# Kernel tuning notes

Hardware: AMD Instinct MI355X
Metric: run time of the kernel (lower is better)

Reference implementation:

```python
import jax, jax.numpy as jnp
import numpy as np

N_NODES = 100000
F_DIM = 128      # graph.num_node_features
TE_DIM = 32      # te_emb_dim
D = F_DIM + TE_DIM  # attention embed_dim = 160
B = 4096         # number of target nodes (batched python loop)
K = 64           # candidates per target
TAU = 1.0
THRESHOLD = 0.2
EPS = 1e-10


def setup_inputs() -> dict:
    key = jax.random.key(0)
    ks = jax.random.split(key, 16)
    inp = {
        "x": jax.random.normal(ks[0], (N_NODES, F_DIM), dtype=jnp.float32),
        "target_node_ids": jax.random.randint(ks[1], (B,), 0, N_NODES),
        "target_node_times": jax.random.randint(ks[2], (B,), 1, 10000),
        "neighbor_ids": jax.random.randint(ks[3], (B, K), 0, N_NODES),
        "edge_time": jax.random.randint(ks[4], (B, K), 0, 10000),
        "edge_weight": jax.random.uniform(ks[5], (B, K), dtype=jnp.float32),
        "gumbel_u": jax.random.uniform(ks[6], (B, K), dtype=jnp.float32),
        # TemporalEncoding params: te(t) = cos(t * w + b)
        "te_w": jax.random.normal(ks[7], (TE_DIM,), dtype=jnp.float32),
        "te_b": jax.random.normal(ks[8], (TE_DIM,), dtype=jnp.float32),
        # MultiheadAttention params (packed qkv like torch)
        "in_proj_w": jax.random.normal(ks[9], (3 * D, D), dtype=jnp.float32) / np.sqrt(D),
        "in_proj_b": jnp.zeros((3 * D,), dtype=jnp.float32),
        "out_w": jax.random.normal(ks[10], (D, D), dtype=jnp.float32) / np.sqrt(D),
        "out_b": jnp.zeros((D,), dtype=jnp.float32),
        # MLP: Linear(D+1 -> 1) + LeakyReLU
        "mlp_w": jax.random.normal(ks[11], (D + 1,), dtype=jnp.float32) / np.sqrt(D + 1),
        "mlp_b": jnp.zeros((1,), dtype=jnp.float32),
    }
    return inp


def reference(x, target_node_ids, target_node_times, neighbor_ids, edge_time,
              edge_weight, gumbel_u, te_w, te_b, in_proj_w, in_proj_b,
              out_w, out_b, mlp_w, mlp_b):
    # --- build target embedding: [B, D]
    t_x = x[target_node_ids]                                          # [B, F]
    t_te = jnp.cos(target_node_times[:, None].astype(jnp.float32) * te_w + te_b)  # [B, TE]
    q_in = jnp.concatenate([t_x, t_te], axis=-1)                      # [B, D]

    # --- candidate embeddings: [B, K, D]
    c_x = x[neighbor_ids]                                             # [B, K, F]
    c_te = jnp.cos(edge_time[..., None].astype(jnp.float32) * te_w + te_b)        # [B, K, TE]
    kv_in = jnp.concatenate([c_x, c_te], axis=-1)                     # [B, K, D]

    # --- single-head MultiheadAttention (eval mode, 1 query per target)
    Wq, Wk, Wv = in_proj_w[:D], in_proj_w[D:2 * D], in_proj_w[2 * D:]
    bq, bk, bv = in_proj_b[:D], in_proj_b[D:2 * D], in_proj_b[2 * D:]
    q = q_in @ Wq.T + bq                                              # [B, D]
    k = jnp.einsum('bkf,df->bkd', kv_in, Wk) + bk                     # [B, K, D]
    v = jnp.einsum('bkf,df->bkd', kv_in, Wv) + bv                     # [B, K, D]
    scores = jnp.einsum('bd,bkd->bk', q, k) / jnp.sqrt(jnp.float32(D))
    attn_w = jax.nn.softmax(scores, axis=-1)                          # [B, K]
    ctx = jnp.einsum('bk,bkd->bd', attn_w, v)                         # [B, D]
    attn_output = ctx @ out_w.T + out_b                               # [B, D]

    # --- gumbel-softmax mask over attention weights (soft, then threshold)
    g = -jnp.log(-jnp.log(gumbel_u + EPS) + EPS)                      # gumbel(0,1)
    y_soft = jax.nn.softmax((attn_w + g) / TAU, axis=-1)
    candidate_mask = y_soft > THRESHOLD                               # [B, K] bool

    # --- MLP edge-weight update: Linear(D+1 -> 1) + LeakyReLU
    mlp_in = jnp.concatenate(
        [jnp.broadcast_to(attn_output[:, None, :], (attn_output.shape[0], edge_weight.shape[1], attn_output.shape[1])),
         edge_weight[..., None]], axis=-1)                            # [B, K, D+1]
    new_edge_weight = jax.nn.leaky_relu(jnp.einsum('bkf,f->bk', mlp_in, mlp_w) + mlp_b[0])  # [B, K]

    return attn_output, new_edge_weight, candidate_mask
```

## Files before the change

### kernel.cpp

```cpp
#include <hip/hip_runtime.h>

#define F_DIM 128
#define TE_DIM 32
#define DD 160
#define NB 4096
#define KK 64
#define ROWS 4
#define LD 164

__device__ __forceinline__ float dot4acc(const float4 w, const float4 v, float a) {
    a = fmaf(w.x, v.x, a);
    a = fmaf(w.y, v.y, a);
    a = fmaf(w.z, v.z, a);
    a = fmaf(w.w, v.w, a);
    return a;
}

__device__ __forceinline__ float wave_max(float v) {
    #pragma unroll
    for (int off = 32; off > 0; off >>= 1) v = fmaxf(v, __shfl_xor(v, off, 64));
    return v;
}
__device__ __forceinline__ float wave_sum(float v) {
    #pragma unroll
    for (int off = 32; off > 0; off >>= 1) v += __shfl_xor(v, off, 64);
    return v;
}

__device__ __forceinline__ void gemv_rows(
    const float* __restrict__ W, const float* __restrict__ bias,
    const float (*vin)[LD], float (*vout)[LD], int tid)
{
    const int r  = tid & 3;
    const int dl = tid >> 2;
    const float4* v4 = (const float4*)vin[r];
    const float4* w0 = (const float4*)(W + (long)dl * DD);
    const float4* w1 = (const float4*)(W + (long)(dl + 64) * DD);
    float a0 = bias[dl];
    float a1 = bias[dl + 64];
    if (dl < 32) {
        const float4* w2 = (const float4*)(W + (long)(dl + 128) * DD);
        float a2 = bias[dl + 128];
        #pragma unroll 8
        for (int f = 0; f < 40; ++f) {
            const float4 v = v4[f];
            a0 = dot4acc(w0[f], v, a0);
            a1 = dot4acc(w1[f], v, a1);
            a2 = dot4acc(w2[f], v, a2);
        }
        vout[r][dl]       = a0;
        vout[r][dl + 64]  = a1;
        vout[r][dl + 128] = a2;
    } else {
        #pragma unroll 8
        for (int f = 0; f < 40; ++f) {
            const float4 v = v4[f];
            a0 = dot4acc(w0[f], v, a0);
            a1 = dot4acc(w1[f], v, a1);
        }
        vout[r][dl]      = a0;
        vout[r][dl + 64] = a1;
    }
}

__global__ __launch_bounds__(256, 4)
void structure_learner_kernel(
    const float* __restrict__ x,
    const int*   __restrict__ target_node_ids,
    const int*   __restrict__ target_node_times,
    const int*   __restrict__ neighbor_ids,
    const int*   __restrict__ edge_time,
    const float* __restrict__ edge_weight,
    const float* __restrict__ gumbel_u,
    const float* __restrict__ te_w,
    const float* __restrict__ te_b,
    const float* __restrict__ in_proj_w,
    const float* __restrict__ in_proj_b,
    const float* __restrict__ out_w,
    const float* __restrict__ out_b,
    const float* __restrict__ mlp_w,
    const float* __restrict__ mlp_b,
    float* __restrict__ out_ao,
    float* __restrict__ out_new,
    float* __restrict__ out_mask)
{
    __shared__ __attribute__((aligned(16))) float s_qin[ROWS][LD];
    __shared__ __attribute__((aligned(16))) float s_q[ROWS][LD];
    __shared__ __attribute__((aligned(16))) float s_qt[ROWS][LD];
    __shared__ __attribute__((aligned(16))) float s_wkv[ROWS][LD];
    __shared__ __attribute__((aligned(16))) float s_ctx[ROWS][LD];
    __shared__ __attribute__((aligned(16))) float s_ao[ROWS][LD];
    __shared__ float s_attnw[ROWS][KK];
    __shared__ float s_sbk[ROWS];
    __shared__ int   s_nid[ROWS][KK];
    __shared__ float s_et[ROWS][KK];

    const int tid  = threadIdx.x;
    const int wr   = tid >> 6;
    const int lane = tid & 63;
    const int b0   = blockIdx.x * ROWS;

    {
        const int b = b0 + wr;
        s_nid[wr][lane] = neighbor_ids[(long)b * KK + lane];
        s_et[wr][lane]  = (float)edge_time[(long)b * KK + lane];
        const int tn = target_node_ids[b];
        const float2 tx = *(const float2*)(x + (long)tn * F_DIM + lane * 2);
        s_qin[wr][lane * 2]     = tx.x;
        s_qin[wr][lane * 2 + 1] = tx.y;
        if (lane < TE_DIM) {
            const float tt = (float)target_node_times[b];
            s_qin[wr][F_DIM + lane] = cosf(tt * te_w[lane] + te_b[lane]);
        }
    }
    __syncthreads();

    gemv_rows(in_proj_w, in_proj_b, s_qin, s_q, tid);
    __syncthreads();

    {
        if (tid < 160) {
            const int r  = tid / 40;
            const int e4 = tid % 40;
            float4 acc = make_float4(0.f, 0.f, 0.f, 0.f);
            const float* qr = s_q[r];
            #pragma unroll 8
            for (int d = 0; d < DD; ++d) {
                const float qd = qr[d];
                const float4 wv = *((const float4*)(in_proj_w + (long)(DD + d) * DD) + e4);
                acc.x = fmaf(qd, wv.x, acc.x);
                acc.y = fmaf(qd, wv.y, acc.y);
                acc.z = fmaf(qd, wv.z, acc.z);
                acc.w = fmaf(qd, wv.w, acc.w);
            }
            *((float4*)s_qt[r] + e4) = acc;
        } else if (tid < 160 + ROWS) {
            const int r = tid - 160;
            float acc = 0.f;
            for (int d = 0; d < DD; ++d)
                acc = fmaf(s_q[r][d], in_proj_b[DD + d], acc);
            s_sbk[r] = acc;
        }
    }
    __syncthreads();

    float my_aw;
    {
        const int r   = wr;
        const int nid = s_nid[r][lane];
        const float et = s_et[r][lane];
        const float4* xr  = (const float4*)(x + (long)nid * F_DIM);
        const float4* qt4 = (const float4*)s_qt[r];
        float acc = 0.f;
        #pragma unroll 8
        for (int f = 0; f < F_DIM / 4; ++f)
            acc = dot4acc(xr[f], qt4[f], acc);
        const float* qtte = s_qt[r] + F_DIM;
        #pragma unroll 8
        for (int j = 0; j < TE_DIM; ++j) {
            const float te = cosf(et * te_w[j] + te_b[j]);
            acc = fmaf(qtte[j], te, acc);
        }
        const float sc = (acc + s_sbk[r]) / sqrtf(160.0f);
        const float m = wave_max(sc);
        const float e = expf(sc - m);
        const float l = wave_sum(e);
        my_aw = e / l;
        s_attnw[r][lane] = my_aw;
    }
    __syncthreads();

    {
        const int r = wr;
        float ax = 0.f, ay = 0.f, at = 0.f;
        const float twl = (lane < TE_DIM) ? te_w[lane] : 0.f;
        const float tbl = (lane < TE_DIM) ? te_b[lane] : 0.f;
        const float* xb = x + lane * 2;
        #pragma unroll 4
        for (int k = 0; k < KK; ++k) {
            const float w   = s_attnw[r][k];
            const int   nid = s_nid[r][k];
            const float2 xv = *(const float2*)(xb + (long)nid * F_DIM);
            ax = fmaf(w, xv.x, ax);
            ay = fmaf(w, xv.y, ay);
            const float te = cosf(s_et[r][k] * twl + tbl);
            at = fmaf(w, te, at);
        }
        s_wkv[r][lane * 2]     = ax;
        s_wkv[r][lane * 2 + 1] = ay;
        if (lane < TE_DIM) s_wkv[r][F_DIM + lane] = at;
    }
    __syncthreads();

    gemv_rows(in_proj_w + (long)2 * DD * DD, in_proj_b + 2 * DD, s_wkv, s_ctx, tid);
    __syncthreads();

    gemv_rows(out_w, out_b, s_ctx, s_ao, tid);
    __syncthreads();

    {
        const int r = wr;
        const int b = b0 + r;
        float p = s_ao[r][lane] * mlp_w[lane];
        p = fmaf(s_ao[r][lane + 64], mlp_w[lane + 64], p);
        if (lane < 32) p = fmaf(s_ao[r][lane + 128], mlp_w[lane + 128], p);
        const float base = wave_sum(p) + mlp_b[0];

        float* ao = out_ao + (long)b * DD;
        ao[lane]      = s_ao[r][lane];
        ao[lane + 64] = s_ao[r][lane + 64];
        if (lane < 32) ao[lane + 128] = s_ao[r][lane + 128];

        const float u = gumbel_u[(long)b * KK + lane];
        const float g = -logf(-logf(u + 1e-10f) + 1e-10f);
        const float z = my_aw + g;
        const float m = wave_max(z);
        const float e = expf(z - m);
        const float l = wave_sum(e);
        const float y = e / l;
        out_mask[(long)b * KK + lane] = (y > 0.2f) ? 1.0f : 0.0f;

        const float ew  = edge_weight[(long)b * KK + lane];
        const float val = fmaf(ew, mlp_w[160], base);
        out_new[(long)b * KK + lane] = (val >= 0.f) ? val : 0.01f * val;
    }
}

extern "C" void kernel_launch(void* const* d_in, const int* in_sizes, int n_in,
                              void* d_out, int out_size, void* d_ws, size_t ws_size,
                              hipStream_t stream) {
    const float* x   = (const float*)d_in[0];
    const int*   tni = (const int*)d_in[1];
    const int*   tnt = (const int*)d_in[2];
    const int*   nid = (const int*)d_in[3];
    const int*   et  = (const int*)d_in[4];
    const float* ew  = (const float*)d_in[5];
    const float* gu  = (const float*)d_in[6];
    const float* tew = (const float*)d_in[7];
    const float* teb = (const float*)d_in[8];
    const float* ipw = (const float*)d_in[9];
    const float* ipb = (const float*)d_in[10];
    const float* ow  = (const float*)d_in[11];
    const float* ob  = (const float*)d_in[12];
    const float* mw  = (const float*)d_in[13];
    const float* mb  = (const float*)d_in[14];

    float* out      = (float*)d_out;
    float* out_ao   = out;
    float* out_new  = out + (long)NB * DD;
    float* out_mask = out + (long)NB * DD + (long)NB * KK;

    dim3 grid(NB / ROWS);
    dim3 block(256);
    structure_learner_kernel<<<grid, block, 0, stream>>>(
        x, tni, tnt, nid, et, ew, gu, tew, teb, ipw, ipb, ow, ob, mw, mb,
        out_ao, out_new, out_mask);
}
```

Before: 192.7 us.

## Precombine attention weight matrices in setup kernel and split rows across two waves

A setup kernel precomputes fused weights: Wq^T·Wk scaled by 1/sqrt(D), Wout·Wv, and the bias-derived vectors and scalar. The main kernel then needs one GEMV for the query-key path and one for the value-output path instead of four chained GEMVs. Each block now handles 2 rows with two waves per row, each wave covering half the candidates. Candidate cosine encodings are computed once into shared memory as fp16 and reused in both the score and context passes. The cost is an extra launch, weights computed from parameters on every call, fp16 rounding of the temporal encodings, and reassociated arithmetic that can shift results slightly.

```diff
diff --git a/kernel.cpp b/kernel.cpp
--- a/kernel.cpp
+++ b/kernel.cpp
@@ -5,8 +5,17 @@
 #define DD 160
 #define NB 4096
 #define KK 64
-#define ROWS 4
+#define ROWS 2
 #define LD 164
+#define TE_STRIDE 36
+
+#define WS_M   0
+#define WS_V2  25600
+#define WS_C   51200
+#define WS_U   51360
+#define WS_B2  51520
+#define WS_S0  51680
+#define WS_TOT 51681
 
 __device__ __forceinline__ float dot4acc(const float4 w, const float4 v, float a) {
     a = fmaf(w.x, v.x, a);
@@ -27,43 +36,49 @@
     return v;
 }
 
-__device__ __forceinline__ void gemv_rows(
-    const float* __restrict__ W, const float* __restrict__ bias,
-    const float (*vin)[LD], float (*vout)[LD], int tid)
+__global__ void setup_kernel(const float* __restrict__ ipw, const float* __restrict__ ipb,
+                             const float* __restrict__ ow,  const float* __restrict__ ob,
+                             float* __restrict__ ws)
 {
-    const int r  = tid & 3;
-    const int dl = tid >> 2;
-    const float4* v4 = (const float4*)vin[r];
-    const float4* w0 = (const float4*)(W + (long)dl * DD);
-    const float4* w1 = (const float4*)(W + (long)(dl + 64) * DD);
-    float a0 = bias[dl];
-    float a1 = bias[dl + 64];
-    if (dl < 32) {
-        const float4* w2 = (const float4*)(W + (long)(dl + 128) * DD);
-        float a2 = bias[dl + 128];
-        #pragma unroll 8
-        for (int f = 0; f < 40; ++f) {
-            const float4 v = v4[f];
-            a0 = dot4acc(w0[f], v, a0);
-            a1 = dot4acc(w1[f], v, a1);
-            a2 = dot4acc(w2[f], v, a2);
-        }
-        vout[r][dl]       = a0;
-        vout[r][dl + 64]  = a1;
-        vout[r][dl + 128] = a2;
-    } else {
-        #pragma unroll 8
-        for (int f = 0; f < 40; ++f) {
-            const float4 v = v4[f];
-            a0 = dot4acc(w0[f], v, a0);
-            a1 = dot4acc(w1[f], v, a1);
-        }
-        vout[r][dl]      = a0;
-        vout[r][dl + 64] = a1;
-    }
-}
-
-__global__ __launch_bounds__(256, 4)
+    const int g = blockIdx.x * blockDim.x + threadIdx.x;
+    const float inv = 0.07905694150420949f;
+    if (g < 25600) {
+        const int e = g / DD, f = g % DD;
+        const float* wk = ipw + DD * DD;
+        float a = 0.f;
+        for (int d = 0; d < DD; ++d) a = fmaf(wk[d * DD + e], ipw[d * DD + f], a);
+        ws[WS_M + g] = a * inv;
+    } else if (g < 51200) {
+        const int gg = g - 25600;
+        const int i = gg / DD, f = gg % DD;
+        const float* wv = ipw + 2 * DD * DD;
+        float a = 0.f;
+        for (int d = 0; d < DD; ++d) a = fmaf(ow[i * DD + d], wv[d * DD + f], a);
+        ws[WS_V2 + gg] = a;
+    } else if (g < 51360) {
+        const int e = g - 51200;
+        const float* wk = ipw + DD * DD;
+        float a = 0.f;
+        for (int d = 0; d < DD; ++d) a = fmaf(wk[d * DD + e], ipb[d], a);
+        ws[WS_C + e] = a * inv;
+    } else if (g < 51520) {
+        const int f = g - 51360;
+        float a = 0.f;
+        for (int d = 0; d < DD; ++d) a = fmaf(ipw[d * DD + f], ipb[DD + d], a);
+        ws[WS_U + f] = a * inv;
+    } else if (g < 51680) {
+        const int i = g - 51520;
+        float a = ob[i];
+        for (int d = 0; d < DD; ++d) a = fmaf(ow[i * DD + d], ipb[2 * DD + d], a);
+        ws[WS_B2 + i] = a;
+    } else if (g == 51680) {
+        float a = 0.f;
+        for (int d = 0; d < DD; ++d) a = fmaf(ipb[d], ipb[DD + d], a);
+        ws[WS_S0] = a * inv;
+    }
+}
+
+__global__ __launch_bounds__(256, 8)
 void structure_learner_kernel(
     const float* __restrict__ x,
     const int*   __restrict__ target_node_ids,
@@ -74,155 +89,198 @@
     const float* __restrict__ gumbel_u,
     const float* __restrict__ te_w,
     const float* __restrict__ te_b,
-    const float* __restrict__ in_proj_w,
-    const float* __restrict__ in_proj_b,
-    const float* __restrict__ out_w,
-    const float* __restrict__ out_b,
     const float* __restrict__ mlp_w,
     const float* __restrict__ mlp_b,
+    const float* __restrict__ ws,
     float* __restrict__ out_ao,
     float* __restrict__ out_new,
     float* __restrict__ out_mask)
 {
     __shared__ __attribute__((aligned(16))) float s_qin[ROWS][LD];
-    __shared__ __attribute__((aligned(16))) float s_q[ROWS][LD];
     __shared__ __attribute__((aligned(16))) float s_qt[ROWS][LD];
-    __shared__ __attribute__((aligned(16))) float s_wkv[ROWS][LD];
-    __shared__ __attribute__((aligned(16))) float s_ctx[ROWS][LD];
+    __shared__ __attribute__((aligned(16))) float s_wkv[ROWS][2][LD];
     __shared__ __attribute__((aligned(16))) float s_ao[ROWS][LD];
+    __shared__ float s_scores[ROWS][KK];
     __shared__ float s_attnw[ROWS][KK];
-    __shared__ float s_sbk[ROWS];
+    __shared__ float s_et[ROWS][KK];
     __shared__ int   s_nid[ROWS][KK];
-    __shared__ float s_et[ROWS][KK];
+    __shared__ _Float16 s_te[ROWS][KK][TE_STRIDE];
 
     const int tid  = threadIdx.x;
-    const int wr   = tid >> 6;
+    const int w    = tid >> 6;
     const int lane = tid & 63;
+    const int r    = w >> 1;
+    const int h    = w & 1;
     const int b0   = blockIdx.x * ROWS;
-
-    {
-        const int b = b0 + wr;
-        s_nid[wr][lane] = neighbor_ids[(long)b * KK + lane];
-        s_et[wr][lane]  = (float)edge_time[(long)b * KK + lane];
+    const int b    = b0 + r;
+
+    const float* Mw = ws + WS_M;
+    const float* V2 = ws + WS_V2;
+    const float* Cv = ws + WS_C;
+    const float* Uv = ws + WS_U;
+    const float* B2 = ws + WS_B2;
+    const float  s0 = ws[WS_S0];
+
+    if (h == 0) {
+        s_nid[r][lane] = neighbor_ids[(long)b * KK + lane];
+        s_et[r][lane]  = (float)edge_time[(long)b * KK + lane];
+    } else {
         const int tn = target_node_ids[b];
         const float2 tx = *(const float2*)(x + (long)tn * F_DIM + lane * 2);
-        s_qin[wr][lane * 2]     = tx.x;
-        s_qin[wr][lane * 2 + 1] = tx.y;
+        s_qin[r][lane * 2]     = tx.x;
+        s_qin[r][lane * 2 + 1] = tx.y;
         if (lane < TE_DIM) {
             const float tt = (float)target_node_times[b];
-            s_qin[wr][F_DIM + lane] = cosf(tt * te_w[lane] + te_b[lane]);
-        }
-    }
-    __syncthreads();
-
-    gemv_rows(in_proj_w, in_proj_b, s_qin, s_q, tid);
-    __syncthreads();
-
-    {
-        if (tid < 160) {
-            const int r  = tid / 40;
-            const int e4 = tid % 40;
-            float4 acc = make_float4(0.f, 0.f, 0.f, 0.f);
-            const float* qr = s_q[r];
+            s_qin[r][F_DIM + lane] = cosf(tt * te_w[lane] + te_b[lane]);
+        }
+    }
+    __syncthreads();
+
+    {
+        const int kl = h * 32 + (lane >> 1);
+        const int fh = lane & 1;
+        const float et = s_et[r][kl];
+        #pragma unroll
+        for (int j = 0; j < 16; ++j) {
+            const int jj = fh * 16 + j;
+            s_te[r][kl][jj] = (_Float16)cosf(et * te_w[jj] + te_b[jj]);
+        }
+    }
+    {
+        const int r2 = tid & 1;
+        const int dl = tid >> 1;
+        const float4* v4 = (const float4*)s_qin[r2];
+        const float4* w0 = (const float4*)(Mw + (long)dl * DD);
+        float a0 = Cv[dl];
+        if (dl < 32) {
+            const float4* w1 = (const float4*)(Mw + (long)(dl + 128) * DD);
+            float a1 = Cv[dl + 128];
             #pragma unroll 8
-            for (int d = 0; d < DD; ++d) {
-                const float qd = qr[d];
-                const float4 wv = *((const float4*)(in_proj_w + (long)(DD + d) * DD) + e4);
-                acc.x = fmaf(qd, wv.x, acc.x);
-                acc.y = fmaf(qd, wv.y, acc.y);
-                acc.z = fmaf(qd, wv.z, acc.z);
-                acc.w = fmaf(qd, wv.w, acc.w);
+            for (int f = 0; f < 40; ++f) {
+                const float4 v = v4[f];
+                a0 = dot4acc(w0[f], v, a0);
+                a1 = dot4acc(w1[f], v, a1);
             }
-            *((float4*)s_qt[r] + e4) = acc;
-        } else if (tid < 160 + ROWS) {
-            const int r = tid - 160;
-            float acc = 0.f;
-            for (int d = 0; d < DD; ++d)
-                acc = fmaf(s_q[r][d], in_proj_b[DD + d], acc);
-            s_sbk[r] = acc;
-        }
-    }
-    __syncthreads();
-
-    float my_aw;
-    {
-        const int r   = wr;
-        const int nid = s_nid[r][lane];
-        const float et = s_et[r][lane];
-        const float4* xr  = (const float4*)(x + (long)nid * F_DIM);
-        const float4* qt4 = (const float4*)s_qt[r];
+            s_qt[r2][dl]       = a0;
+            s_qt[r2][dl + 128] = a1;
+        } else {
+            #pragma unroll 8
+            for (int f = 0; f < 40; ++f) {
+                const float4 v = v4[f];
+                a0 = dot4acc(w0[f], v, a0);
+            }
+            s_qt[r2][dl] = a0;
+        }
+    }
+    __syncthreads();
+
+    {
+        float p = s_qin[r][lane] * Uv[lane];
+        p = fmaf(s_qin[r][lane + 64], Uv[lane + 64], p);
+        if (lane < 32) p = fmaf(s_qin[r][128 + lane], Uv[128 + lane], p);
+        const float sbk = wave_sum(p) + s0;
+
+        const int kl = h * 32 + (lane >> 1);
+        const int fh = lane & 1;
+        const int nid = s_nid[r][kl];
+        const float4* xr  = (const float4*)(x + (long)nid * F_DIM + fh * 64);
+        const float4* qt4 = (const float4*)(s_qt[r] + fh * 64);
         float acc = 0.f;
-        #pragma unroll 8
-        for (int f = 0; f < F_DIM / 4; ++f)
-            acc = dot4acc(xr[f], qt4[f], acc);
-        const float* qtte = s_qt[r] + F_DIM;
-        #pragma unroll 8
-        for (int j = 0; j < TE_DIM; ++j) {
-            const float te = cosf(et * te_w[j] + te_b[j]);
-            acc = fmaf(qtte[j], te, acc);
-        }
-        const float sc = (acc + s_sbk[r]) / sqrtf(160.0f);
+        #pragma unroll
+        for (int f = 0; f < 16; ++f) acc = dot4acc(xr[f], qt4[f], acc);
+        const float* qte = s_qt[r] + F_DIM + fh * 16;
+        const _Float16* te = &s_te[r][kl][fh * 16];
+        #pragma unroll
+        for (int j = 0; j < 16; ++j) acc = fmaf(qte[j], (float)te[j], acc);
+        acc += __shfl_xor(acc, 1, 64);
+        if (fh == 0) s_scores[r][kl] = acc + sbk;
+    }
+    __syncthreads();
+
+    float aw;
+    {
+        const float sc = s_scores[r][lane];
         const float m = wave_max(sc);
         const float e = expf(sc - m);
         const float l = wave_sum(e);
-        my_aw = e / l;
-        s_attnw[r][lane] = my_aw;
-    }
-    __syncthreads();
-
-    {
-        const int r = wr;
+        aw = e / l;
+        if (h == 0) s_attnw[r][lane] = aw;
+    }
+    __syncthreads();
+
+    {
         float ax = 0.f, ay = 0.f, at = 0.f;
-        const float twl = (lane < TE_DIM) ? te_w[lane] : 0.f;
-        const float tbl = (lane < TE_DIM) ? te_b[lane] : 0.f;
         const float* xb = x + lane * 2;
+        const int kbase = h * 32;
         #pragma unroll 4
-        for (int k = 0; k < KK; ++k) {
-            const float w   = s_attnw[r][k];
+        for (int kk = 0; kk < 32; ++kk) {
+            const int k = kbase + kk;
+            const float wgt = s_attnw[r][k];
             const int   nid = s_nid[r][k];
             const float2 xv = *(const float2*)(xb + (long)nid * F_DIM);
-            ax = fmaf(w, xv.x, ax);
-            ay = fmaf(w, xv.y, ay);
-            const float te = cosf(s_et[r][k] * twl + tbl);
-            at = fmaf(w, te, at);
-        }
-        s_wkv[r][lane * 2]     = ax;
-        s_wkv[r][lane * 2 + 1] = ay;
-        if (lane < TE_DIM) s_wkv[r][F_DIM + lane] = at;
-    }
-    __syncthreads();
-
-    gemv_rows(in_proj_w + (long)2 * DD * DD, in_proj_b + 2 * DD, s_wkv, s_ctx, tid);
-    __syncthreads();
-
-    gemv_rows(out_w, out_b, s_ctx, s_ao, tid);
-    __syncthreads();
-
-    {
-        const int r = wr;
-        const int b = b0 + r;
+            ax = fmaf(wgt, xv.x, ax);
+            ay = fmaf(wgt, xv.y, ay);
+            if (lane < TE_DIM) at = fmaf(wgt, (float)s_te[r][k][lane], at);
+        }
+        s_wkv[r][h][lane * 2]     = ax;
+        s_wkv[r][h][lane * 2 + 1] = ay;
+        if (lane < TE_DIM) s_wkv[r][h][F_DIM + lane] = at;
+    }
+    __syncthreads();
+
+    {
+        const int r2 = tid & 1;
+        const int dl = tid >> 1;
+        const float4* va = (const float4*)s_wkv[r2][0];
+        const float4* vb = (const float4*)s_wkv[r2][1];
+        const float4* w0 = (const float4*)(V2 + (long)dl * DD);
+        float a0 = B2[dl];
+        if (dl < 32) {
+            const float4* w1 = (const float4*)(V2 + (long)(dl + 128) * DD);
+            float a1 = B2[dl + 128];
+            #pragma unroll 8
+            for (int f = 0; f < 40; ++f) {
+                const float4 p = va[f], q = vb[f];
+                const float4 v = make_float4(p.x + q.x, p.y + q.y, p.z + q.z, p.w + q.w);
+                a0 = dot4acc(w0[f], v, a0);
+                a1 = dot4acc(w1[f], v, a1);
+            }
+            s_ao[r2][dl]       = a0;
+            s_ao[r2][dl + 128] = a1;
+        } else {
+            #pragma unroll 8
+            for (int f = 0; f < 40; ++f) {
+                const float4 p = va[f], q = vb[f];
+                const float4 v = make_float4(p.x + q.x, p.y + q.y, p.z + q.z, p.w + q.w);
+                a0 = dot4acc(w0[f], v, a0);
+            }
+            s_ao[r2][dl] = a0;
+        }
+    }
+    __syncthreads();
+
+    if (h == 0) {
         float p = s_ao[r][lane] * mlp_w[lane];
         p = fmaf(s_ao[r][lane + 64], mlp_w[lane + 64], p);
         if (lane < 32) p = fmaf(s_ao[r][lane + 128], mlp_w[lane + 128], p);
         const float base = wave_sum(p) + mlp_b[0];
 
+        const float u = gumbel_u[(long)b * KK + lane];
+        const float g = -logf(-logf(u + 1e-10f) + 1e-10f);
+        const float z = aw + g;
+        const float m = wave_max(z);
+        const float e = expf(z - m);
+        const float l = wave_sum(e);
+        out_mask[(long)b * KK + lane] = (e / l > 0.2f) ? 1.0f : 0.0f;
+
+        const float ew  = edge_weight[(long)b * KK + lane];
+        const float val = fmaf(ew, mlp_w[DD], base);
+        out_new[(long)b * KK + lane] = (val >= 0.f) ? val : 0.01f * val;
+    } else {
         float* ao = out_ao + (long)b * DD;
         ao[lane]      = s_ao[r][lane];
         ao[lane + 64] = s_ao[r][lane + 64];
         if (lane < 32) ao[lane + 128] = s_ao[r][lane + 128];
-
-        const float u = gumbel_u[(long)b * KK + lane];
-        const float g = -logf(-logf(u + 1e-10f) + 1e-10f);
-        const float z = my_aw + g;
-        const float m = wave_max(z);
-        const float e = expf(z - m);
-        const float l = wave_sum(e);
-        const float y = e / l;
-        out_mask[(long)b * KK + lane] = (y > 0.2f) ? 1.0f : 0.0f;
-
-        const float ew  = edge_weight[(long)b * KK + lane];
-        const float val = fmaf(ew, mlp_w[160], base);
-        out_new[(long)b * KK + lane] = (val >= 0.f) ? val : 0.01f * val;
     }
 }
 
@@ -245,14 +303,16 @@
     const float* mw  = (const float*)d_in[13];
     const float* mb  = (const float*)d_in[14];
 
+    float* wsf = (float*)d_ws;
+
     float* out      = (float*)d_out;
     float* out_ao   = out;
     float* out_new  = out + (long)NB * DD;
     float* out_mask = out + (long)NB * DD + (long)NB * KK;
 
-    dim3 grid(NB / ROWS);
-    dim3 block(256);
-    structure_learner_kernel<<<grid, block, 0, stream>>>(
-        x, tni, tnt, nid, et, ew, gu, tew, teb, ipw, ipb, ow, ob, mw, mb,
+    setup_kernel<<<(WS_TOT + 255) / 256, 256, 0, stream>>>(ipw, ipb, ow, ob, wsf);
+
+    structure_learner_kernel<<<NB / ROWS, 256, 0, stream>>>(
+        x, tni, tnt, nid, et, ew, gu, tew, teb, mw, mb, wsf,
         out_ao, out_new, out_mask);
 }
```

Measured after the change: 243.0 us. +26.1%, slower.
